# Kernel tuning notes

Measured on AMD Instinct MI355X. Metric: run time of the kernel, lower is better.

## Reference

```python
import jax, jax.numpy as jnp
import numpy as np

THRESHOLD = 0.6
SCALE = 1.0


def _tffix(mat):
    # floor for >=0, ceil for <0 (round toward zero)
    return jnp.where(mat >= 0, jnp.floor(mat), jnp.ceil(mat))


def _rec2square(rect):
    # rect: [N,5] = x1,y1,x2,y2,score -> square boxes, same center-ish rule as original
    x1, y1, x2, y2, s = rect[:, 0], rect[:, 1], rect[:, 2], rect[:, 3], rect[:, 4]
    w = x2 - x1
    h = y2 - y1
    l = jnp.maximum(w, h)
    nx1 = x1 + w * 0.5 - l * 0.5
    ny1 = y1 + h * 0.5 - l * 0.5
    return jnp.stack([nx1, ny1, nx1 + l, ny1 + l, s], axis=-1)


def _post_single(cls_el, roi_el):
    # cls_el: [H,W,2], roi_el: [H,W,4]
    H, W = cls_el.shape[0], cls_el.shape[1]
    # Cls_pro = transpose(classifier[...,1:2], [1,0,2]) -> prob[w,h]
    prob = cls_el[:, :, 1].T                      # [W,H]
    roi = jnp.transpose(roi_el, (2, 1, 0))        # [4,W,H]
    out_side = max(W, H)                          # static shapes -> python scalar
    stride = ((2 * out_side + 11 - 12) / (out_side - 1)) if (2 * out_side != 11) else 0.0
    stride = jnp.float32(stride)
    # all grid positions in row-major order over [W,H] (matches tf.where ordering)
    wi, hi = jnp.meshgrid(jnp.arange(W), jnp.arange(H), indexing='ij')
    bb = jnp.stack([wi, hi], axis=-1).astype(jnp.float32).reshape(-1, 2)   # [WH,2]
    bb1 = _tffix(stride * bb)
    bb2 = _tffix(stride * bb + 11.0)
    offset = roi.reshape(4, -1).T                 # [WH,4] = dx1..dx4 per position
    box = jnp.concatenate([bb1, bb2], axis=-1) + offset * 12.0 * SCALE      # [WH,4]
    score = prob.reshape(-1, 1)                   # [WH,1]
    rect = _rec2square(jnp.concatenate([box, score], axis=-1))              # [WH,5]
    # fixed-shape compaction of the tf.where(prob>=thr) selection:
    mask = prob.reshape(-1) >= THRESHOLD
    order = jnp.argsort(jnp.logical_not(mask), stable=True)  # valid rows first, stable
    rect = rect[order] * mask[order][:, None].astype(rect.dtype)            # pad rows = 0
    return rect


def setup_inputs() -> dict:
    key = jax.random.key(0)
    k1, k2 = jax.random.split(key)
    B, H, W = 16, 540, 960
    classifier = jax.random.uniform(k1, (B, H, W, 2), dtype=jnp.float32)
    bbox_regress = jax.random.normal(k2, (B, H, W, 4), dtype=jnp.float32)
    img_shape = jnp.ones((B, 2), dtype=jnp.float32)
    return {"classifier": classifier, "bbox_regress": bbox_regress, "img_shape": img_shape}


def reference(classifier, bbox_regress, img_shape):
    rect = jax.vmap(_post_single)(classifier, bbox_regress)   # [B, H*W, 5]
    return (rect, rect, img_shape + 1.0)
```

## Files before the change

kernel.cpp:

```cpp
#include <hip/hip_runtime.h>

#define HH 540
#define WW 960
#define NB 16
#define NPB (HH * WW)
#define NF  (NPB * 5)
static const float STRIDE_F = (float)(1919.0 / 959.0);
#define THR 0.6f

__global__ void k_zero(int* __restrict__ p, int n) {
    int i = blockIdx.x * blockDim.x + threadIdx.x;
    if (i < n) p[i] = 0;
}

__global__ void k_count(const float* __restrict__ cls, int* __restrict__ colcnt) {
    int w = blockIdx.x * 256 + threadIdx.x;
    int b = blockIdx.z;
    int h0 = blockIdx.y * 54;
    if (w >= WW) return;
    const float* base = cls + (size_t)b * NPB * 2;
    int c = 0;
    for (int h = h0; h < h0 + 54; ++h)
        c += (base[(size_t)(h * WW + w) * 2 + 1] >= THR) ? 1 : 0;
    if (c) atomicAdd(&colcnt[b * WW + w], c);
}

__global__ void k_scan(const int* __restrict__ colcnt, int* __restrict__ colbase,
                       int* __restrict__ totals, const float* __restrict__ img,
                       float* __restrict__ out_img) {
    __shared__ int s[1024];
    int b = blockIdx.x;
    int t = threadIdx.x;
    int v = (t < WW) ? colcnt[b * WW + t] : 0;
    s[t] = v;
    __syncthreads();
    for (int d = 1; d < 1024; d <<= 1) {
        int x = s[t];
        int y = (t >= d) ? s[t - d] : 0;
        __syncthreads();
        s[t] = x + y;
        __syncthreads();
    }
    if (t < WW) colbase[b * WW + t] = s[t] - v;
    if (t == 0) totals[b] = s[1023];
    if (t < 2) out_img[b * 2 + t] = img[b * 2 + t] + 1.0f;
}

__global__ __launch_bounds__(256) void k_compact(const float* __restrict__ cls,
                                                 const float4* __restrict__ roi,
                                                 const int* __restrict__ colbase,
                                                 float* __restrict__ out1,
                                                 float* __restrict__ out2) {
    __shared__ int msk[16][16];
    int t = threadIdx.x;
    int w_l = t & 15;
    int h_l = t >> 4;
    int b = blockIdx.y;
    int w = blockIdx.x * 16 + w_l;
    const float*  cbase = cls + (size_t)b * NPB * 2;
    const float4* rbase = roi + (size_t)b * NPB;
    int cb  = colbase[b * WW + w];
    int run = 0;
    float sxw = truncf(STRIDE_F * (float)w);
    float exw = truncf(STRIDE_F * (float)w + 11.0f);
    for (int ih = 0; ih < 34; ++ih) {
        int h = ih * 16 + h_l;
        bool valid = h < HH;
        float p = 0.0f;
        float4 r = make_float4(0.f, 0.f, 0.f, 0.f);
        if (valid) {
            p = cbase[(size_t)(h * WW + w) * 2 + 1];
            r = rbase[h * WW + w];
        }
        int m = (valid && p >= THR) ? 1 : 0;
        __syncthreads();
        msk[h_l][w_l] = m;
        __syncthreads();
        int off = 0, tot = 0;
#pragma unroll
        for (int i = 0; i < 16; ++i) {
            int v = msk[i][w_l];
            tot += v;
            if (i < h_l) off += v;
        }
        if (m) {
            float sy = truncf(STRIDE_F * (float)h);
            float ey = truncf(STRIDE_F * (float)h + 11.0f);
            float x1 = sxw + r.x * 12.0f;
            float y1 = sy  + r.y * 12.0f;
            float x2 = exw + r.z * 12.0f;
            float y2 = ey  + r.w * 12.0f;
            float wd = x2 - x1;
            float hd = y2 - y1;
            float l  = fmaxf(wd, hd);
            float nx1 = x1 + wd * 0.5f - l * 0.5f;
            float ny1 = y1 + hd * 0.5f - l * 0.5f;
            int pos = cb + run + off;
            size_t o = ((size_t)b * NPB + (size_t)pos) * 5;
            out1[o + 0] = nx1; out1[o + 1] = ny1; out1[o + 2] = nx1 + l;
            out1[o + 3] = ny1 + l; out1[o + 4] = p;
            out2[o + 0] = nx1; out2[o + 1] = ny1; out2[o + 2] = nx1 + l;
            out2[o + 3] = ny1 + l; out2[o + 4] = p;
        }
        run += tot;
    }
}

__global__ void k_ztail(const int* __restrict__ totals, float* __restrict__ out1,
                        float* __restrict__ out2) {
    int b = blockIdx.y;
    int K5 = totals[b] * 5;
    int chunk = blockIdx.x * blockDim.x + threadIdx.x;
    int f0 = chunk * 4;
    if (f0 >= NF) return;
    size_t base = (size_t)b * NF;
    if (f0 >= K5) {
        float4 z = make_float4(0.f, 0.f, 0.f, 0.f);
        *(float4*)(out1 + base + f0) = z;
        *(float4*)(out2 + base + f0) = z;
    } else if (f0 + 4 > K5) {
        for (int j = K5; j < f0 + 4; ++j) {
            out1[base + j] = 0.0f;
            out2[base + j] = 0.0f;
        }
    }
}

extern "C" void kernel_launch(void* const* d_in, const int* in_sizes, int n_in,
                              void* d_out, int out_size, void* d_ws, size_t ws_size,
                              hipStream_t stream) {
    const float* cls = (const float*)d_in[0];
    const float* roi = (const float*)d_in[1];
    const float* img = (const float*)d_in[2];

    float* out1 = (float*)d_out;
    float* out2 = out1 + (size_t)NB * NF;
    float* outimg = out2 + (size_t)NB * NF;

    int* colcnt  = (int*)d_ws;
    int* colbase = colcnt + NB * WW;
    int* totals  = colbase + NB * WW;

    k_zero<<<dim3((NB * WW + 255) / 256), dim3(256), 0, stream>>>(colcnt, NB * WW);
    k_count<<<dim3(4, 10, NB), dim3(256), 0, stream>>>(cls, colcnt);
    k_scan<<<dim3(NB), dim3(1024), 0, stream>>>(colcnt, colbase, totals, img, outimg);
    k_compact<<<dim3(60, NB), dim3(256), 0, stream>>>(cls, (const float4*)roi, colbase,
                                                      out1, out2);
    k_ztail<<<dim3((NF / 4 + 255) / 256, NB), dim3(256), 0, stream>>>(totals, out1, out2);
}
```

Baseline: 540.8 us.

## Stage compacted rows in LDS and use wave ballots for column offsets

The count kernel now reads float4 pairs so each thread handles two columns, which halves the number of load instructions. The compact kernel replaces the shared-memory mask scan with wave ballot plus popcount prefix sums. It loads the ROI only for selected positions, then stages the output rows in LDS so that 16 threads per column write contiguous runs of the output. This is meant to turn scattered 5-float stores into more coalesced ones, at the cost of an extra __syncthreads per iteration and LDS traffic.

```diff
diff --git a/kernel.cpp b/kernel.cpp
--- a/kernel.cpp
+++ b/kernel.cpp
@@ -13,16 +13,21 @@
     if (i < n) p[i] = 0;
 }
 
-__global__ void k_count(const float* __restrict__ cls, int* __restrict__ colcnt) {
-    int w = blockIdx.x * 256 + threadIdx.x;
+__global__ void k_count(const float4* __restrict__ cls4, int* __restrict__ colcnt) {
+    int tw = blockIdx.x * 256 + threadIdx.x;
     int b = blockIdx.z;
     int h0 = blockIdx.y * 54;
-    if (w >= WW) return;
-    const float* base = cls + (size_t)b * NPB * 2;
-    int c = 0;
-    for (int h = h0; h < h0 + 54; ++h)
-        c += (base[(size_t)(h * WW + w) * 2 + 1] >= THR) ? 1 : 0;
-    if (c) atomicAdd(&colcnt[b * WW + w], c);
+    if (tw >= WW / 2) return;
+    int w0 = tw * 2;
+    const float4* base = cls4 + (size_t)b * (NPB / 2);
+    int c0 = 0, c1 = 0;
+    for (int h = h0; h < h0 + 54; ++h) {
+        float4 v = base[(size_t)(h * WW + w0) >> 1];
+        c0 += (v.y >= THR) ? 1 : 0;
+        c1 += (v.w >= THR) ? 1 : 0;
+    }
+    if (c0) atomicAdd(&colcnt[b * WW + w0], c0);
+    if (c1) atomicAdd(&colcnt[b * WW + w0 + 1], c1);
 }
 
 __global__ void k_scan(const int* __restrict__ colcnt, int* __restrict__ colbase,
@@ -51,39 +56,50 @@
                                                  const int* __restrict__ colbase,
                                                  float* __restrict__ out1,
                                                  float* __restrict__ out2) {
-    __shared__ int msk[16][16];
+    __shared__ int wcnt_s[4][16];
+    __shared__ float rows_s[16 * 80];
     int t = threadIdx.x;
     int w_l = t & 15;
     int h_l = t >> 4;
+    int wave = t >> 6;
+    int h_lw = h_l & 3;
     int b = blockIdx.y;
     int w = blockIdx.x * 16 + w_l;
     const float*  cbase = cls + (size_t)b * NPB * 2;
     const float4* rbase = roi + (size_t)b * NPB;
-    int cb  = colbase[b * WW + w];
-    int run = 0;
+
+    int fc = h_l;
+    int fj = w_l;
+    int cb_f = colbase[b * WW + blockIdx.x * 16 + fc];
+    int run_f = 0;
+
     float sxw = truncf(STRIDE_F * (float)w);
     float exw = truncf(STRIDE_F * (float)w + 11.0f);
+
     for (int ih = 0; ih < 34; ++ih) {
         int h = ih * 16 + h_l;
         bool valid = h < HH;
-        float p = 0.0f;
-        float4 r = make_float4(0.f, 0.f, 0.f, 0.f);
-        if (valid) {
-            p = cbase[(size_t)(h * WW + w) * 2 + 1];
-            r = rbase[h * WW + w];
+        float p = valid ? cbase[(size_t)(h * WW + w) * 2 + 1] : 0.0f;
+        bool m = valid && (p >= THR);
+
+        unsigned long long bal = __ballot(m);
+        unsigned long long colmask = 0x0001000100010001ULL << w_l;
+        int off_w = __popcll(bal & colmask & ((1ULL << (h_lw * 16)) - 1ULL));
+        int wc    = __popcll(bal & colmask);
+
+        __syncthreads();
+        if (h_lw == 0) wcnt_s[wave][w_l] = wc;
+        __syncthreads();
+
+        int off = off_w;
+#pragma unroll
+        for (int v = 0; v < 4; ++v) {
+            int x = wcnt_s[v][w_l];
+            if (v < wave) off += x;
         }
-        int m = (valid && p >= THR) ? 1 : 0;
-        __syncthreads();
-        msk[h_l][w_l] = m;
-        __syncthreads();
-        int off = 0, tot = 0;
-#pragma unroll
-        for (int i = 0; i < 16; ++i) {
-            int v = msk[i][w_l];
-            tot += v;
-            if (i < h_l) off += v;
-        }
+
         if (m) {
+            float4 r = rbase[h * WW + w];
             float sy = truncf(STRIDE_F * (float)h);
             float ey = truncf(STRIDE_F * (float)h + 11.0f);
             float x1 = sxw + r.x * 12.0f;
@@ -95,14 +111,24 @@
             float l  = fmaxf(wd, hd);
             float nx1 = x1 + wd * 0.5f - l * 0.5f;
             float ny1 = y1 + hd * 0.5f - l * 0.5f;
-            int pos = cb + run + off;
-            size_t o = ((size_t)b * NPB + (size_t)pos) * 5;
-            out1[o + 0] = nx1; out1[o + 1] = ny1; out1[o + 2] = nx1 + l;
-            out1[o + 3] = ny1 + l; out1[o + 4] = p;
-            out2[o + 0] = nx1; out2[o + 1] = ny1; out2[o + 2] = nx1 + l;
-            out2[o + 3] = ny1 + l; out2[o + 4] = p;
+            int sb = w_l * 80 + off * 5;
+            rows_s[sb + 0] = nx1;
+            rows_s[sb + 1] = ny1;
+            rows_s[sb + 2] = nx1 + l;
+            rows_s[sb + 3] = ny1 + l;
+            rows_s[sb + 4] = p;
         }
-        run += tot;
+        __syncthreads();
+
+        int tot_f = wcnt_s[0][fc] + wcnt_s[1][fc] + wcnt_s[2][fc] + wcnt_s[3][fc];
+        int nd = tot_f * 5;
+        size_t gb = ((size_t)b * NPB + (size_t)(cb_f + run_f)) * 5;
+        for (int d = fj; d < nd; d += 16) {
+            float val = rows_s[fc * 80 + d];
+            out1[gb + d] = val;
+            out2[gb + d] = val;
+        }
+        run_f += tot_f;
     }
 }
 
@@ -142,7 +168,7 @@
     int* totals  = colbase + NB * WW;
 
     k_zero<<<dim3((NB * WW + 255) / 256), dim3(256), 0, stream>>>(colcnt, NB * WW);
-    k_count<<<dim3(4, 10, NB), dim3(256), 0, stream>>>(cls, colcnt);
+    k_count<<<dim3(2, 10, NB), dim3(256), 0, stream>>>((const float4*)cls, colcnt);
     k_scan<<<dim3(NB), dim3(1024), 0, stream>>>(colcnt, colbase, totals, img, outimg);
     k_compact<<<dim3(60, NB), dim3(256), 0, stream>>>(cls, (const float4*)roi, colbase,
                                                       out1, out2);
```

Result: faster. 517.0 us (-4.4%).
